# Optimization experiments

Measured on AMD Instinct MI355X. Metric: run time of the kernel, lower is better.

The kernel has to match this reference:

```python
import jax, jax.numpy as jnp
import numpy as np

E = 512
H = 8
D = E // H
WIN = 128  # mask_window_size


def setup_inputs() -> dict:
    key = jax.random.key(0)
    k1, k2, k3, k4, k5 = jax.random.split(key, 5)
    B, L = 2, 4096
    s = 1.0 / np.sqrt(E)
    return {
        "x": jax.random.normal(k1, (B, L, E), dtype=jnp.float32),
        "in_proj_w": jax.random.normal(k2, (3 * E, E), dtype=jnp.float32) * s,
        "in_proj_b": jax.random.normal(k3, (3 * E,), dtype=jnp.float32) * 0.02,
        "out_w": jax.random.normal(k4, (E, E), dtype=jnp.float32) * s,
        "out_b": jax.random.normal(k5, (E,), dtype=jnp.float32) * 0.02,
    }


def reference(x, in_proj_w, in_proj_b, out_w, out_b):
    B, L, _ = x.shape
    # fused qkv projection (torch MultiheadAttention in_proj): x @ W.T + b
    qkv = jnp.einsum("ble,fe->blf", x, in_proj_w) + in_proj_b  # [B,L,3E]
    q, k, v = jnp.split(qkv, 3, axis=-1)
    # [B,H,L,D]
    q = q.reshape(B, L, H, D).transpose(0, 2, 1, 3)
    k = k.reshape(B, L, H, D).transpose(0, 2, 1, 3)
    v = v.reshape(B, L, H, D).transpose(0, 2, 1, 3)
    scores = jnp.einsum("bhqd,bhkd->bhqk", q, k) / jnp.sqrt(jnp.float32(D))
    # (diagonal stays blocked — faithful to the original gen_mask quirk)
    idx = jnp.arange(L)
    dist = jnp.abs(idx[:, None] - idx[None, :])
    blocked = (dist > WIN) | (dist == 0)  # [L,L]
    scores = jnp.where(blocked[None, None], -jnp.inf, scores)
    attn = jax.nn.softmax(scores, axis=-1)  # [B,H,L,L]
    out = jnp.einsum("bhqk,bhkd->bhqd", attn, v)  # [B,H,L,D]
    out = out.transpose(0, 2, 1, 3).reshape(B, L, E)
    return jnp.einsum("ble,fe->blf", out, out_w) + out_b
```

## Files before the change

kernel.cpp:

```cpp
#include <hip/hip_runtime.h>
#include <math.h>

#define E_DIM 512
#define H_DIM 8
#define WIN 128
#define L_SEQ 4096
#define B_SZ 2

typedef unsigned short ushort_t;
typedef unsigned int uint_t;
typedef __attribute__((ext_vector_type(8))) __bf16 bf16x8;
typedef __attribute__((ext_vector_type(4))) float f32x4;

__device__ __forceinline__ ushort_t f2bf(float f) {
    uint_t u = __float_as_uint(f);
    u = u + 0x7fffu + ((u >> 16) & 1u);
    return (ushort_t)(u >> 16);
}
__device__ __forceinline__ uint_t pk2bf(float lo, float hi) {
    uint_t r;
    asm("v_cvt_pk_bf16_f32 %0, %1, %2" : "=v"(r) : "v"(lo), "v"(hi));
    return r;
}

__device__ __forceinline__ void gload16(const ushort_t* g, ushort_t* l) {
    __builtin_amdgcn_global_load_lds(
        (const __attribute__((address_space(1))) void*)g,
        (__attribute__((address_space(3))) void*)l,
        16, 0, 0);
}


__global__ __launch_bounds__(256) void convertX(
    const float* __restrict__ x,  ushort_t* __restrict__ xh,
    const float* __restrict__ w1, ushort_t* __restrict__ w1h,
    const float* __restrict__ w2, ushort_t* __restrict__ w2h) {
    int sg = blockIdx.x * 256 + threadIdx.x;
    const float* src; ushort_t* dh;
    if (sg < 524288)      { src = x;  dh = xh; }
    else if (sg < 622592) { src = w1; dh = w1h; sg -= 524288; }
    else                  { src = w2; dh = w2h; sg -= 622592; }
    const int tile = sg >> 6, slot = sg & 63;
    const int row = (tile >> 4) * 16 + (slot & 15);
    const int k   = (tile & 15) * 32 + (slot >> 4) * 8;
    const float4 v0 = *(const float4*)&src[(size_t)row * 512 + k];
    const float4 v1 = *(const float4*)&src[(size_t)row * 512 + k + 4];
    uint4 ov;
    ov.x = pk2bf(v0.x, v0.y);
    ov.y = pk2bf(v0.z, v0.w);
    ov.z = pk2bf(v1.x, v1.y);
    ov.w = pk2bf(v1.z, v1.w);
    *(uint4*)(dh + (size_t)sg * 8) = ov;
}

__global__ __launch_bounds__(256) void gemm_qkv(
    const ushort_t* __restrict__ Ah,
    const ushort_t* __restrict__ Wh,
    const float* __restrict__ bias,
    ushort_t* __restrict__ qTh,
    ushort_t* __restrict__ kTh,
    ushort_t* __restrict__ vTh) {
    __shared__ __align__(16) ushort_t sAh[3][8 * 512];
    __shared__ __align__(16) ushort_t sWh[3][8 * 512];

    const int tid = threadIdx.x, lane = tid & 63, w = tid >> 6;
    const int wm = w & 1, wn = w >> 1, ln = lane & 15, quad = lane >> 4;
    const int bx = blockIdx.x, by = blockIdx.y;
    const int lo8 = lane * 8;
    const int wu = __builtin_amdgcn_readfirstlane(w);

    const ushort_t* sA0 = &sAh[0][0];
    const ushort_t* sW0 = &sWh[0][0];
    const int BUF = 8 * 512;

    f32x4 acc[4][4];
    const f32x4 zero = {0.f, 0.f, 0.f, 0.f};
    #pragma unroll
    for (int i = 0; i < 4; i++)
        #pragma unroll
        for (int j = 0; j < 4; j++) acc[i][j] = zero;

    const ushort_t* pb[4];
    ushort_t* db[4];
    #pragma unroll
    for (int t = 0; t < 4; t++) {
        const int g = wu * 4 + t;
        if (g < 8) {
            pb[t] = Ah + ((size_t)(bx * 8 + g) * 16) * 512;
            db[t] = &sAh[0][g * 512];
        } else {
            const int u = g - 8;
            pb[t] = Wh + ((size_t)(by * 8 + u) * 16) * 512;
            db[t] = &sWh[0][u * 512];
        }
    }

    #pragma unroll
    for (int t = 0; t < 4; t++) gload16(pb[t] + lo8, db[t]);
    #pragma unroll
    for (int t = 0; t < 4; t++) gload16(pb[t] + 512 + lo8, db[t] + BUF);

    int bw = 2, br = 0;
    for (int kt = 0; kt < 16; kt++) {
        if (kt < 15) asm volatile("s_waitcnt vmcnt(4) lgkmcnt(0)" ::: "memory");
        else         asm volatile("s_waitcnt vmcnt(0) lgkmcnt(0)" ::: "memory");
        __builtin_amdgcn_s_barrier();
        __builtin_amdgcn_sched_barrier(0);

        if (kt < 14) {
            const int koff = (kt + 2) * 512;
            const int bwo = bw * BUF;
            #pragma unroll
            for (int t = 0; t < 4; t++)
                gload16(pb[t] + koff + lo8, db[t] + bwo);
            bw = (bw == 2) ? 0 : bw + 1;
        }

        const int bro = br * BUF;
        br = (br == 2) ? 0 : br + 1;

        bf16x8 fah[4];
        #pragma unroll
        for (int i = 0; i < 4; i++)
            fah[i] = *(const bf16x8*)&sA0[bro + (wm * 4 + i) * 512 + lo8];
        #pragma unroll
        for (int j = 0; j < 4; j++) {
            const bf16x8 fbh = *(const bf16x8*)&sW0[bro + (wn * 4 + j) * 512 + lo8];
            #pragma unroll
            for (int i = 0; i < 4; i++)
                acc[i][j] = __builtin_amdgcn_mfma_f32_16x16x32_bf16(fah[i], fbh, acc[i][j], 0, 0, 0);
        }
    }

    const int b = bx >> 5;
    const int h = 2 * (by & 3) + wn;
    if (by < 8) {
        ushort_t* dh = (by < 4) ? qTh : kTh;
        #pragma unroll
        for (int i = 0; i < 4; i++) {
            const int rt = (bx & 31) * 8 + wm * 4 + i;
            const size_t tb = ((size_t)(b * 8 + h) * 256 + rt) * 2;
            #pragma unroll
            for (int j = 0; j < 4; j++) {
                const float bv = bias[by * 128 + wn * 64 + j * 16 + ln];
                const size_t tile = tb + (j >> 1);
                const uint_t pa = pk2bf(acc[i][j][0] + bv, acc[i][j][1] + bv);
                const uint_t pc = pk2bf(acc[i][j][2] + bv, acc[i][j][3] + bv);
                const int slot0 = ((j * 2 + (ln >> 3)) & 3) * 16 + quad * 4;
                const size_t idx0 = tile * 512 + slot0 * 8 + (ln & 7);
                dh[idx0]      = (ushort_t)pa;
                dh[idx0 + 8]  = (ushort_t)(pa >> 16);
                dh[idx0 + 16] = (ushort_t)pc;
                dh[idx0 + 24] = (ushort_t)(pc >> 16);
            }
        }
    } else {
        const int kwin = (bx & 31) * 2 + wm;
        #pragma unroll
        for (int i = 0; i < 4; i++) {
            const int kk = i >> 1;
            #pragma unroll
            for (int j = 0; j < 4; j++) {
                const float bv = bias[by * 128 + wn * 64 + j * 16 + ln];
                const size_t tile = (((size_t)(b * 8 + h) * 64 + kwin) * 4 + j) * 2 + kk;
                const uint_t pa = pk2bf(acc[i][j][0] + bv, acc[i][j][1] + bv);
                const uint_t pc = pk2bf(acc[i][j][2] + bv, acc[i][j][3] + bv);
                const int slot = ((i & 1) * 2 + (quad >> 1)) * 16 + ln;
                uint2 ov; ov.x = pa; ov.y = pc;
                *(uint2*)&vTh[tile * 512 + slot * 8 + (quad & 1) * 4] = ov;
            }
        }
    }
}

__global__ __launch_bounds__(512) void attn_mfma(
    const ushort_t* __restrict__ qTh,
    const ushort_t* __restrict__ kTh,
    const ushort_t* __restrict__ vTh,
    ushort_t* __restrict__ outh) {
    __shared__ __align__(16) ushort_t sKh[2][8 * 512];
    __shared__ __align__(16) ushort_t sV [2][8 * 512];
    __shared__ __align__(16) ushort_t sP [16 * 512];

    const int qs = blockIdx.x * 128;
    const int h = blockIdx.y, b = blockIdx.z;
    const int bh = b * 8 + h;
    const int tid = threadIdx.x, lane = tid & 63;
    const int w = tid >> 6, ln = lane & 15, quad = lane >> 4;
    const int lo8 = lane * 8;

    bf16x8 qf[2];
    {
        const size_t qt = ((size_t)bh * 256 + (qs >> 4) + w) * 2;
        qf[0] = *(const bf16x8*)(qTh + (qt + 0) * 512 + lo8);
        qf[1] = *(const bf16x8*)(qTh + (qt + 1) * 512 + lo8);
    }

    f32x4 oacc[4];
    const f32x4 zero = {0.f, 0.f, 0.f, 0.f};
    #pragma unroll
    for (int dt = 0; dt < 4; dt++) oacc[dt] = zero;
    float m_run = -1e30f, l_run = 0.f;

    const float cscale = 0.125f * 1.44269504f;
    const int qlo = qs + 16 * w;
    const int q = qlo + ln;
    const int lo_b = (q - WIN) < 0 ? 0 : (q - WIN);
    const int hi_b = (q + WIN) > (L_SEQ - 1) ? (L_SEQ - 1) : (q + WIN);

    {
        if (w < 4) {
            int st = (qs >> 4) - 8 + w;
            st = st < 0 ? 0 : (st > 255 ? 255 : st);
            const size_t kb = ((size_t)bh * 256 + st) * 2 * 512 + lo8;
            gload16(kTh + kb,       &sKh[0][(w * 2 + 0) * 512]);
            gload16(kTh + kb + 512, &sKh[0][(w * 2 + 1) * 512]);
        } else {
            const int u = w - 4;
            int vw = (qs >> 6) - 2;
            vw = vw < 0 ? 0 : (vw > 63 ? 63 : vw);
            const size_t vb = (((size_t)bh * 64 + vw) * 4 + u) * 2 * 512 + lo8;
            gload16(vTh + vb,       &sV[0][(u * 2 + 0) * 512]);
            gload16(vTh + vb + 512, &sV[0][(u * 2 + 1) * 512]);
        }
    }

    for (int kt = 0; kt < 6; kt++) {
        const int ks = qs - 128 + kt * 64;

        __syncthreads();

        if (kt < 5) {
            const int nb = (kt + 1) & 1;
            if (w < 4) {
                int st = (qs >> 4) - 8 + (kt + 1) * 4 + w;
                st = st < 0 ? 0 : (st > 255 ? 255 : st);
                const size_t kb = ((size_t)bh * 256 + st) * 2 * 512 + lo8;
                gload16(kTh + kb,       &sKh[nb][(w * 2 + 0) * 512]);
                gload16(kTh + kb + 512, &sKh[nb][(w * 2 + 1) * 512]);
            } else {
                const int u = w - 4;
                int vw = (qs >> 6) - 2 + kt + 1;
                vw = vw < 0 ? 0 : (vw > 63 ? 63 : vw);
                const size_t vb = (((size_t)bh * 64 + vw) * 4 + u) * 2 * 512 + lo8;
                gload16(vTh + vb,       &sV[nb][(u * 2 + 0) * 512]);
                gload16(vTh + vb + 512, &sV[nb][(u * 2 + 1) * 512]);
            }
        }
        const int cb = kt & 1;

        bool dead[4];
        #pragma unroll
        for (int jt = 0; jt < 4; jt++) {
            const int klo = ks + 16 * jt;
            dead[jt] = (klo > qlo + 15 + WIN) || (klo + 15 < qlo - WIN) ||
                       (klo >= L_SEQ) || (klo + 15 < 0);
        }
        const bool hdead0 = dead[0] && dead[1];
        const bool hdead1 = dead[2] && dead[3];
        const bool ktAlive = !(hdead0 && hdead1);

        if (ktAlive) {
            f32x4 st4[4];
            __builtin_amdgcn_s_setprio(1);
            #pragma unroll
            for (int jt = 0; jt < 4; jt++) {
                f32x4 a = zero;
                if (!dead[jt]) {
                    #pragma unroll
                    for (int kk = 0; kk < 2; kk++) {
                        const bf16x8 kh = *(const bf16x8*)&sKh[cb][(jt * 2 + kk) * 512 + lo8];
                        a = __builtin_amdgcn_mfma_f32_16x16x32_bf16(kh, qf[kk], a, 0, 0, 0);
                    }
                }
                st4[jt] = a;
            }
            __builtin_amdgcn_s_setprio(0);

            float mkr = -INFINITY;
            #pragma unroll
            for (int jt = 0; jt < 4; jt++)
                if (!dead[jt])
                    #pragma unroll
                    for (int r = 0; r < 4; r++)
                        mkr = fmaxf(mkr, st4[jt][r]);
            mkr = fmaxf(mkr, __shfl_xor(mkr, 16));
            mkr = fmaxf(mkr, __shfl_xor(mkr, 32));

            const float mnew = fmaxf(m_run, mkr * cscale);
            const bool raised = mnew > m_run;
            const float alpha = exp2f(m_run - mnew);
            m_run = mnew;

            float ps = 0.f;
            #pragma unroll
            for (int jt = 0; jt < 4; jt++) {
                if (!dead[jt]) {
                    #pragma unroll
                    for (int r = 0; r < 4; r++) {
                        const int kcol = ks + jt * 16 + quad * 4 + r;
                        const bool ok = (kcol >= lo_b) && (kcol <= hi_b) && (kcol != q);
                        float p = exp2f(st4[jt][r] * cscale - mnew);
                        p = ok ? p : 0.f;
                        st4[jt][r] = p;
                        ps += p;
                    }
                }
            }
            ps += __shfl_xor(ps, 16);
            ps += __shfl_xor(ps, 32);
            l_run = l_run * alpha + ps;

            if (__any(raised)) {
                float ar[4];
                #pragma unroll
                for (int r = 0; r < 4; r++)
                    ar[r] = __shfl(alpha, quad * 4 + r);
                #pragma unroll
                for (int dt = 0; dt < 4; dt++)
                    #pragma unroll
                    for (int r = 0; r < 4; r++)
                        oacc[dt][r] *= ar[r];
            }

            #pragma unroll
            for (int jt = 0; jt < 4; jt++) {
                const bool hd = (jt < 2) ? hdead0 : hdead1;
                if (!hd) {
                    uint2 pw;
                    if (!dead[jt]) {
                        pw.x = pk2bf(st4[jt][0], st4[jt][1]);
                        pw.y = pk2bf(st4[jt][2], st4[jt][3]);
                    } else { pw.x = 0u; pw.y = 0u; }
                    const int slot = ((jt & 1) * 2 + (quad >> 1)) * 16 + ln;
                    *(uint2*)&sP[w * 1024 + (jt >> 1) * 512 + slot * 8 + (quad & 1) * 4] = pw;
                }
            }

            #pragma unroll
            for (int kk = 0; kk < 2; kk++) {
                const bool hd = (kk == 0) ? hdead0 : hdead1;
                if (!hd) {
                    const bf16x8 pf = *(const bf16x8*)&sP[w * 1024 + kk * 512 + lo8];
                    __builtin_amdgcn_s_setprio(1);
                    #pragma unroll
                    for (int dt = 0; dt < 4; dt++) {
                        const bf16x8 vf = *(const bf16x8*)&sV[cb][(dt * 2 + kk) * 512 + lo8];
                        oacc[dt] = __builtin_amdgcn_mfma_f32_16x16x32_bf16(pf, vf, oacc[dt], 0, 0, 0);
                    }
                    __builtin_amdgcn_s_setprio(0);
                }
            }
        }
    }

    const int Rt = ((b * L_SEQ + qs) >> 4) + w;
    float invl[4];
    #pragma unroll
    for (int r = 0; r < 4; r++) {
        const float lr = __shfl(l_run, quad * 4 + r);
        invl[r] = __builtin_amdgcn_rcpf(lr);
    }
    #pragma unroll
    for (int dt = 0; dt < 4; dt++) {
        const uint_t pa = pk2bf(oacc[dt][0] * invl[0], oacc[dt][1] * invl[1]);
        const uint_t pc = pk2bf(oacc[dt][2] * invl[2], oacc[dt][3] * invl[3]);
        const int tile = Rt * 16 + h * 2 + (dt >> 1);
        const int slot0 = ((dt & 1) * 2 + (ln >> 3)) * 16 + quad * 4;
        const size_t idx0 = (size_t)tile * 512 + slot0 * 8 + (ln & 7);
        outh[idx0]      = (ushort_t)pa;
        outh[idx0 + 8]  = (ushort_t)(pa >> 16);
        outh[idx0 + 16] = (ushort_t)pc;
        outh[idx0 + 24] = (ushort_t)(pc >> 16);
    }
}

__global__ __launch_bounds__(512) void gemm_out(
    const ushort_t* __restrict__ Ah,
    const ushort_t* __restrict__ Wh,
    const float* __restrict__ bias, float* __restrict__ C) {
    __shared__ __align__(16) ushort_t sAh[3][16 * 512];
    __shared__ __align__(16) ushort_t sWh[3][8 * 512];

    const int tid = threadIdx.x, lane = tid & 63, w = tid >> 6;
    const int wm = w & 3, wn = w >> 2, ln = lane & 15, quad = lane >> 4;
    const int bx = blockIdx.x, by = blockIdx.y;
    const int lo8 = lane * 8;
    const int wu = __builtin_amdgcn_readfirstlane(w);

    const ushort_t* sA0 = &sAh[0][0];
    const ushort_t* sW0 = &sWh[0][0];
    const int BUFA = 16 * 512, BUFW = 8 * 512;

    f32x4 acc[2][2];
    const f32x4 zero = {0.f, 0.f, 0.f, 0.f};
    #pragma unroll
    for (int i = 0; i < 2; i++)
        #pragma unroll
        for (int j = 0; j < 2; j++) acc[i][j] = zero;

    const ushort_t* pb[3];
    ushort_t* db[3];
    int ds[3];
    #pragma unroll
    for (int t = 0; t < 3; t++) {
        const int g = wu * 3 + t;
        if (g < 16) {
            pb[t] = Ah + ((size_t)(bx * 8 + (g >> 1)) * 16 + (g & 1)) * 512;
            db[t] = &sAh[0][g * 512]; ds[t] = BUFA;
        } else {
            const int u = g - 16;
            pb[t] = Wh + ((size_t)(by * 4 + (u >> 1)) * 16 + (u & 1)) * 512;
            db[t] = &sWh[0][u * 512]; ds[t] = BUFW;
        }
    }

    #pragma unroll
    for (int t = 0; t < 3; t++) gload16(pb[t] + lo8, db[t]);
    #pragma unroll
    for (int t = 0; t < 3; t++) gload16(pb[t] + 1024 + lo8, db[t] + ds[t]);

    int bw = 2, br = 0;
    for (int KT = 0; KT < 8; KT++) {
        if (KT < 7) asm volatile("s_waitcnt vmcnt(3) lgkmcnt(0)" ::: "memory");
        else        asm volatile("s_waitcnt vmcnt(0) lgkmcnt(0)" ::: "memory");
        __builtin_amdgcn_s_barrier();
        __builtin_amdgcn_sched_barrier(0);

        if (KT < 6) {
            const int koff = (KT + 2) * 1024;
            #pragma unroll
            for (int t = 0; t < 3; t++)
                gload16(pb[t] + koff + lo8, db[t] + bw * ds[t]);
            bw = (bw == 2) ? 0 : bw + 1;
        }

        const int broA = br * BUFA, broW = br * BUFW;
        br = (br == 2) ? 0 : br + 1;

        #pragma unroll
        for (int ks = 0; ks < 2; ks++) {
            bf16x8 fah[2];
            #pragma unroll
            for (int i = 0; i < 2; i++)
                fah[i] = *(const bf16x8*)&sA0[broA + ((wm * 2 + i) * 2 + ks) * 512 + lo8];
            #pragma unroll
            for (int j = 0; j < 2; j++) {
                const bf16x8 fbh = *(const bf16x8*)&sW0[broW + ((wn * 2 + j) * 2 + ks) * 512 + lo8];
                #pragma unroll
                for (int i = 0; i < 2; i++)
                    acc[i][j] = __builtin_amdgcn_mfma_f32_16x16x32_bf16(fah[i], fbh, acc[i][j], 0, 0, 0);
            }
        }
    }

    #pragma unroll
    for (int i = 0; i < 2; i++) {
        const int row0 = bx * 128 + wm * 32 + i * 16 + quad * 4;
        #pragma unroll
        for (int j = 0; j < 2; j++) {
            const int col = by * 64 + wn * 32 + j * 16 + ln;
            const float bv = bias[col];
            #pragma unroll
            for (int r = 0; r < 4; r++)
                C[(size_t)(row0 + r) * E_DIM + col] = acc[i][j][r] + bv;
        }
    }
}

extern "C" void kernel_launch(void* const* d_in, const int* in_sizes, int n_in,
                              void* d_out, int out_size, void* d_ws, size_t ws_size,
                              hipStream_t stream) {
    const float* x         = (const float*)d_in[0];
    const float* in_proj_w = (const float*)d_in[1];
    const float* in_proj_b = (const float*)d_in[2];
    const float* out_w     = (const float*)d_in[3];
    const float* out_b     = (const float*)d_in[4];
    float* out = (float*)d_out;

    const int N = B_SZ * L_SEQ;
    const size_t NE = (size_t)N * E_DIM;

    char* p = (char*)d_ws;
    ushort_t* xh  = (ushort_t*)p; p += NE * 2;
    ushort_t* w1h = (ushort_t*)p; p += (size_t)3 * E_DIM * E_DIM * 2;
    ushort_t* w2h = (ushort_t*)p; p += (size_t)E_DIM * E_DIM * 2;
    ushort_t* qTh = (ushort_t*)p; p += NE * 2;
    ushort_t* kTh = (ushort_t*)p; p += NE * 2;
    ushort_t* vTh = (ushort_t*)p; p += NE * 2;
    ushort_t* ath = (ushort_t*)p; p += NE * 2;

    convertX<<<2560, 256, 0, stream>>>(x, xh, in_proj_w, w1h, out_w, w2h);

    gemm_qkv<<<dim3(64, 12), 256, 0, stream>>>(
        xh, w1h, in_proj_b, qTh, kTh, vTh);

    attn_mfma<<<dim3(L_SEQ / 128, H_DIM, B_SZ), 512, 0, stream>>>(
        qTh, kTh, vTh, ath);

    gemm_out<<<dim3(64, 8), 512, 0, stream>>>(
        ath, w2h, out_b, out);
}
```

Baseline: 127.1 us.

## Triple-buffer K/V loads and use lazy softmax rescaling with deferred row-sum reduction

The attention kernel moves from double to triple buffering of the K and V tiles, with explicit vmcnt waits and a raw barrier so two tiles are in flight at once. Online softmax now rescales the running max only when a new score exceeds the current max by more than a threshold (8 in log2 units), so the per-step cross-lane max and sum shuffles disappear. The row sum is kept per lane and reduced once at the end. This costs more LDS per block, which may lower occupancy, and the lazy max relies on bounded exponent growth staying inside fp32 range.

```diff
diff --git a/kernel.cpp b/kernel.cpp
--- a/kernel.cpp
+++ b/kernel.cpp
@@ -178,8 +178,8 @@
     const ushort_t* __restrict__ kTh,
     const ushort_t* __restrict__ vTh,
     ushort_t* __restrict__ outh) {
-    __shared__ __align__(16) ushort_t sKh[2][8 * 512];
-    __shared__ __align__(16) ushort_t sV [2][8 * 512];
+    __shared__ __align__(16) ushort_t sKh[3][8 * 512];
+    __shared__ __align__(16) ushort_t sV [3][8 * 512];
     __shared__ __align__(16) ushort_t sP [16 * 512];
 
     const int qs = blockIdx.x * 128;
@@ -200,7 +200,7 @@
     const f32x4 zero = {0.f, 0.f, 0.f, 0.f};
     #pragma unroll
     for (int dt = 0; dt < 4; dt++) oacc[dt] = zero;
-    float m_run = -1e30f, l_run = 0.f;
+    float m_run = -1e30f, l_loc = 0.f;
 
     const float cscale = 0.125f * 1.44269504f;
     const int qlo = qs + 16 * w;
@@ -208,46 +208,37 @@
     const int lo_b = (q - WIN) < 0 ? 0 : (q - WIN);
     const int hi_b = (q + WIN) > (L_SEQ - 1) ? (L_SEQ - 1) : (q + WIN);
 
-    {
+    auto stage = [&](int t, int bi) {
         if (w < 4) {
-            int st = (qs >> 4) - 8 + w;
+            int st = (qs >> 4) - 8 + t * 4 + w;
             st = st < 0 ? 0 : (st > 255 ? 255 : st);
             const size_t kb = ((size_t)bh * 256 + st) * 2 * 512 + lo8;
-            gload16(kTh + kb,       &sKh[0][(w * 2 + 0) * 512]);
-            gload16(kTh + kb + 512, &sKh[0][(w * 2 + 1) * 512]);
+            gload16(kTh + kb,       &sKh[bi][(w * 2 + 0) * 512]);
+            gload16(kTh + kb + 512, &sKh[bi][(w * 2 + 1) * 512]);
         } else {
             const int u = w - 4;
-            int vw = (qs >> 6) - 2;
+            int vw = (qs >> 6) - 2 + t;
             vw = vw < 0 ? 0 : (vw > 63 ? 63 : vw);
             const size_t vb = (((size_t)bh * 64 + vw) * 4 + u) * 2 * 512 + lo8;
-            gload16(vTh + vb,       &sV[0][(u * 2 + 0) * 512]);
-            gload16(vTh + vb + 512, &sV[0][(u * 2 + 1) * 512]);
-        }
-    }
-
+            gload16(vTh + vb,       &sV[bi][(u * 2 + 0) * 512]);
+            gload16(vTh + vb + 512, &sV[bi][(u * 2 + 1) * 512]);
+        }
+    };
+
+    stage(0, 0);
+    stage(1, 1);
+
+    #pragma unroll
     for (int kt = 0; kt < 6; kt++) {
         const int ks = qs - 128 + kt * 64;
 
-        __syncthreads();
-
-        if (kt < 5) {
-            const int nb = (kt + 1) & 1;
-            if (w < 4) {
-                int st = (qs >> 4) - 8 + (kt + 1) * 4 + w;
-                st = st < 0 ? 0 : (st > 255 ? 255 : st);
-                const size_t kb = ((size_t)bh * 256 + st) * 2 * 512 + lo8;
-                gload16(kTh + kb,       &sKh[nb][(w * 2 + 0) * 512]);
-                gload16(kTh + kb + 512, &sKh[nb][(w * 2 + 1) * 512]);
-            } else {
-                const int u = w - 4;
-                int vw = (qs >> 6) - 2 + kt + 1;
-                vw = vw < 0 ? 0 : (vw > 63 ? 63 : vw);
-                const size_t vb = (((size_t)bh * 64 + vw) * 4 + u) * 2 * 512 + lo8;
-                gload16(vTh + vb,       &sV[nb][(u * 2 + 0) * 512]);
-                gload16(vTh + vb + 512, &sV[nb][(u * 2 + 1) * 512]);
-            }
-        }
-        const int cb = kt & 1;
+        if (kt < 5) asm volatile("s_waitcnt vmcnt(2) lgkmcnt(0)" ::: "memory");
+        else        asm volatile("s_waitcnt vmcnt(0) lgkmcnt(0)" ::: "memory");
+        __builtin_amdgcn_s_barrier();
+        __builtin_amdgcn_sched_barrier(0);
+
+        if (kt < 4) stage(kt + 2, (kt + 2) % 3);
+        const int cb = kt % 3;
 
         bool dead[4];
         #pragma unroll
@@ -277,41 +268,22 @@
             }
             __builtin_amdgcn_s_setprio(0);
 
-            float mkr = -INFINITY;
+            float lmax = -INFINITY;
             #pragma unroll
             for (int jt = 0; jt < 4; jt++)
                 if (!dead[jt])
                     #pragma unroll
                     for (int r = 0; r < 4; r++)
-                        mkr = fmaxf(mkr, st4[jt][r]);
-            mkr = fmaxf(mkr, __shfl_xor(mkr, 16));
-            mkr = fmaxf(mkr, __shfl_xor(mkr, 32));
-
-            const float mnew = fmaxf(m_run, mkr * cscale);
-            const bool raised = mnew > m_run;
-            const float alpha = exp2f(m_run - mnew);
-            m_run = mnew;
-
-            float ps = 0.f;
-            #pragma unroll
-            for (int jt = 0; jt < 4; jt++) {
-                if (!dead[jt]) {
-                    #pragma unroll
-                    for (int r = 0; r < 4; r++) {
-                        const int kcol = ks + jt * 16 + quad * 4 + r;
-                        const bool ok = (kcol >= lo_b) && (kcol <= hi_b) && (kcol != q);
-                        float p = exp2f(st4[jt][r] * cscale - mnew);
-                        p = ok ? p : 0.f;
-                        st4[jt][r] = p;
-                        ps += p;
-                    }
-                }
-            }
-            ps += __shfl_xor(ps, 16);
-            ps += __shfl_xor(ps, 32);
-            l_run = l_run * alpha + ps;
-
-            if (__any(raised)) {
+                        lmax = fmaxf(lmax, st4[jt][r]);
+
+            const bool trig = __any(lmax * cscale > m_run + 8.f);
+            if (trig) {
+                float mk = fmaxf(lmax, __shfl_xor(lmax, 16));
+                mk = fmaxf(mk, __shfl_xor(mk, 32));
+                const float mnew = fmaxf(m_run, mk * cscale);
+                const float alpha = exp2f(m_run - mnew);
+                m_run = mnew;
+                l_loc *= alpha;
                 float ar[4];
                 #pragma unroll
                 for (int r = 0; r < 4; r++)
@@ -321,6 +293,21 @@
                     #pragma unroll
                     for (int r = 0; r < 4; r++)
                         oacc[dt][r] *= ar[r];
+            }
+
+            #pragma unroll
+            for (int jt = 0; jt < 4; jt++) {
+                if (!dead[jt]) {
+                    #pragma unroll
+                    for (int r = 0; r < 4; r++) {
+                        const int kcol = ks + jt * 16 + quad * 4 + r;
+                        const bool ok = (kcol >= lo_b) && (kcol <= hi_b) && (kcol != q);
+                        float p = exp2f(st4[jt][r] * cscale - m_run);
+                        p = ok ? p : 0.f;
+                        st4[jt][r] = p;
+                        l_loc += p;
+                    }
+                }
             }
 
             #pragma unroll
@@ -354,11 +341,14 @@
         }
     }
 
+    float ls = l_loc;
+    ls += __shfl_xor(ls, 16);
+    ls += __shfl_xor(ls, 32);
     const int Rt = ((b * L_SEQ + qs) >> 4) + w;
     float invl[4];
     #pragma unroll
     for (int r = 0; r < 4; r++) {
-        const float lr = __shfl(l_run, quad * 4 + r);
+        const float lr = __shfl(ls, quad * 4 + r);
         invl[r] = __builtin_amdgcn_rcpf(lr);
     }
     #pragma unroll
```

After: 126.6 us. No clear change (-0.4%).
